# Performance work log

Measured on AMD Instinct MI355X. Metric: run time of the kernel, lower is better.

## Reference

```python
import jax, jax.numpy as jnp
import numpy as np

N = 16384      # nodes
E = 262144     # edges (avg degree 16)
H = 128        # hidden_channels
F = 128        # num_filters
G = 50         # num_gaussians
L = 6          # num_interactions
NG = 16        # graphs in batch
CUTOFF = 10.0
BOX = 5.0
LN2 = 0.6931471805599453


def _ssp(x):  # ShiftedSoftplus
    return jax.nn.softplus(x) - LN2


def setup_inputs() -> dict:
    key = jax.random.key(0)
    ks = jax.random.split(key, 20)
    w = lambda k, shape: jax.random.normal(k, shape, dtype=jnp.float32) * 0.1
    return {
        "z": jax.random.randint(ks[0], (N,), 0, 2),
        "pos": jax.random.uniform(ks[1], (N, 3), dtype=jnp.float32) * BOX,
        "edge_index": jax.random.randint(ks[2], (2, E), 0, N),
        "batch": jnp.sort(jax.random.randint(ks[3], (N,), 0, NG)),
        "emb": w(ks[4], (2, H)),
        "mlp_w1": w(ks[5], (L, G, F)),
        "mlp_b1": jnp.zeros((L, F), jnp.float32),
        "mlp_w2": w(ks[6], (L, F, F)),
        "mlp_b2": jnp.zeros((L, F), jnp.float32),
        "cf_w1": w(ks[7], (L, H, F)),
        "cf_w2": w(ks[8], (L, F, H)),
        "cf_b2": jnp.zeros((L, H), jnp.float32),
        "lin_w": w(ks[9], (L, H, H)),
        "lin_b": jnp.zeros((L, H), jnp.float32),
        "out_w1": w(ks[10], (H, H // 2)),
        "out_b1": jnp.zeros((H // 2,), jnp.float32),
        "out_w2": w(ks[11], (H // 2, 1)),
        "out_b2": jnp.zeros((1,), jnp.float32),
    }


def reference(z, pos, edge_index, batch, emb, mlp_w1, mlp_b1, mlp_w2, mlp_b2,
              cf_w1, cf_w2, cf_b2, lin_w, lin_b, out_w1, out_b1, out_w2, out_b2):
    row, col = edge_index[0], edge_index[1]  # message flows row -> col
    dx = pos[row] - pos[col]
    dx = dx - jnp.round(dx / BOX) * BOX      # minimum-image PBC
    ew = jnp.sqrt(jnp.sum(dx * dx, axis=-1))               # [E]
    offset = jnp.linspace(0.0, CUTOFF, G)
    coeff = -0.5 / (offset[1] - offset[0]) ** 2
    ea = jnp.exp(coeff * (ew[:, None] - offset[None, :]) ** 2)  # [E, G]
    C = 0.5 * (jnp.cos(ew * jnp.pi / CUTOFF) + 1.0)
    C = C * (ew < CUTOFF).astype(C.dtype)                   # [E]

    h = emb[z]                                              # [N, H]
    for l in range(L):
        # continuous filter from smeared distances, with cosine cutoff
        W = (_ssp(ea @ mlp_w1[l] + mlp_b1[l]) @ mlp_w2[l] + mlp_b2[l]) * C[:, None]  # [E, F]
        xh = h @ cf_w1[l]                                   # [N, F] (lin1, no bias)
        msg = xh[row] * W                                   # gather x_j, modulate
        agg = jax.ops.segment_sum(msg, col, num_segments=N)  # scatter-add
        xc = agg @ cf_w2[l] + cf_b2[l]                      # [N, H] (lin2)
        h = h + (_ssp(xc) @ lin_w[l] + lin_b[l])            # residual interaction

    h = _ssp(h @ out_w1 + out_b1) @ out_w2 + out_b2         # [N, 1]
    out = jax.ops.segment_sum(h, batch, num_segments=NG)    # readout 'add'
    return jax.nn.sigmoid(out)                              # [NG, 1]
```

## Files before the change

### kernel.cpp

```cpp
#include <hip/hip_runtime.h>
#include <math.h>

#define N_NODES 16384
#define N_EDGES 262144
#define HDIM    128
#define NG50    50
#define NLAYER  6
#define NGRAPH  16
#define TROWS   1025
#define RMAXF   4.34f
#define WPL     16384

__device__ __forceinline__ float ssp_f(float x){
  return (x > 20.0f ? x : log1pf(__expf(x))) - 0.6931471805599453f;
}
__device__ __forceinline__ void fma4(float4& c, float a, const float4 b){
  c.x = fmaf(a,b.x,c.x); c.y = fmaf(a,b.y,c.y); c.z = fmaf(a,b.z,c.z); c.w = fmaf(a,b.w,c.w);
}
__device__ __forceinline__ unsigned short f2bf(float x){
  unsigned u = __float_as_uint(x);
  u += 0x7FFF + ((u>>16)&1);
  return (unsigned short)(u>>16);
}
__device__ __forceinline__ float bf2f(unsigned short u){
  return __uint_as_float(((unsigned)u)<<16);
}

typedef __attribute__((ext_vector_type(8))) short bf16x8;
typedef __attribute__((ext_vector_type(4))) float f32x4;
__device__ __forceinline__ int swzf(int lin){ return lin ^ (((lin>>9)&7)<<4); }

__device__ __forceinline__ void split8(const float4 v0, const float4 v1, bf16x8& hi, bf16x8& lo){
  float x[8] = {v0.x,v0.y,v0.z,v0.w,v1.x,v1.y,v1.z,v1.w};
  #pragma unroll
  for (int i=0;i<8;++i){
    unsigned short h = f2bf(x[i]);
    hi[i] = (short)h;
    lo[i] = (short)f2bf(x[i] - bf2f(h));
  }
}

#define TAB_R   4
#define TAB_NB  257
#define B_INIT  2048
#define B_TAB   1542
#define B_HIST  1024
#define B_WPACK 144
#define K1_GRID (B_INIT + B_TAB + B_HIST + B_WPACK)

__global__ __launch_bounds__(256) void k_setup1(
    const int* __restrict__ z, const float* __restrict__ emb, float* __restrict__ h,
    const float* __restrict__ w1, const float* __restrict__ b1,
    const float* __restrict__ w2, const float* __restrict__ b2, float* __restrict__ tab,
    const int* __restrict__ ei, int* __restrict__ cursor,
    const float* __restrict__ cf_w2, const float* __restrict__ lin_w,
    const float* __restrict__ cf_w1, ushort* __restrict__ wp)
{
  __shared__ float ea[TAB_R][52];
  __shared__ float sT[TAB_R][HDIM];
  __shared__ float part[2][TAB_R][HDIM];
  const int b = blockIdx.x;
  const int tid = threadIdx.x;

  if (b < B_INIT){
    int t = b*256 + tid;
    int n = t >> 5, q = t & 31;
    ((float4*)h)[t] = ((const float4*)emb)[(z[n]<<5) + q];
    return;
  }
  if (b < B_INIT + B_TAB){
    int bb = b - B_INIT;
    int l  = bb / TAB_NB;
    int i0 = (bb % TAB_NB) * TAB_R;
    int j    = tid & 127;
    int half = tid >> 7;
    const float* w1l = w1 + (size_t)l*NG50*HDIM;
    const float* w2l = w2 + (size_t)l*HDIM*HDIM;
    float* tabl = tab + (size_t)l*TROWS*HDIM;
    const float STEP = RMAXF/1024.0f;
    const float GS   = 10.0f/49.0f;
    const float GC   = -0.5f/(GS*GS);
    if (tid < TAB_R*NG50){
      int rr = tid / NG50, k = tid - rr*NG50;
      int ri = i0 + rr; if (ri > TROWS-1) ri = TROWS-1;
      float d = ri*STEP - k*GS;
      ea[rr][k] = __expf(GC*d*d);
    }
    __syncthreads();
    {
      float acc[TAB_R] = {0,0,0,0};
      int kb = half*25;
      for (int k=0;k<25;++k){
        float wv = w1l[(kb+k)*HDIM + j];
        #pragma unroll
        for (int r=0;r<TAB_R;++r) acc[r] = fmaf(ea[r][kb+k], wv, acc[r]);
      }
      #pragma unroll
      for (int r=0;r<TAB_R;++r) part[half][r][j] = acc[r];
    }
    __syncthreads();
    {
      float b1v = b1[(size_t)l*HDIM + j];
      #pragma unroll
      for (int rr=0;rr<2;++rr){
        int r = half*2 + rr;
        sT[r][j] = ssp_f(part[0][r][j] + part[1][r][j] + b1v);
      }
    }
    __syncthreads();
    {
      float o[TAB_R] = {0,0,0,0};
      int kb = half*64;
      #pragma unroll 4
      for (int k=0;k<64;++k){
        float wv = w2l[(kb+k)*HDIM + j];
        #pragma unroll
        for (int r=0;r<TAB_R;++r) o[r] = fmaf(sT[r][kb+k], wv, o[r]);
      }
      #pragma unroll
      for (int r=0;r<TAB_R;++r) part[half][r][j] = o[r];
    }
    __syncthreads();
    {
      float b2v = b2[(size_t)l*HDIM + j];
      #pragma unroll
      for (int rr=0;rr<2;++rr){
        int r = half*2 + rr;
        int ri = i0 + r;
        if (ri < TROWS){
          float rv = ri*STEP;
          float C = 0.5f*(cosf(rv*0.31415926535897931f) + 1.0f);
          tabl[(size_t)ri*HDIM + j] = (part[0][r][j] + part[1][r][j] + b2v)*C;
        }
      }
    }
    return;
  }
  if (b < B_INIT + B_TAB + B_HIST){
    int e = (b - (B_INIT + B_TAB))*256 + tid;
    if (e < N_EDGES) atomicAdd(&cursor[ei[N_EDGES + e]], 1);
    return;
  }
  {
    int bb  = b - (B_INIT + B_TAB + B_HIST);
    int mat = bb >> 3;
    int s   = (bb & 7)*256 + tid;
    const float* M = (mat < 6)  ? cf_w2 + (size_t)mat*HDIM*HDIM
                   : (mat < 12) ? lin_w + (size_t)(mat-6)*HDIM*HDIM
                                : cf_w1 + (size_t)(mat-12)*HDIM*HDIM;
    int ct = s >> 8, ks = (s >> 6) & 3, l = s & 63;
    int col = ct*16 + (l & 15);
    int r0  = ks*32 + (l >> 4)*8;
    ushort oh[8], ol[8];
    #pragma unroll
    for (int i=0;i<8;++i){
      float w = M[(size_t)(r0+i)*HDIM + col];
      oh[i] = f2bf(w);
      ol[i] = f2bf(w - bf2f(oh[i]));
    }
    ushort* dh = wp + (size_t)(2*mat)*WPL + (size_t)s*8;
    ushort* dl = dh + WPL;
    *(ushort4*)(dh+0) = make_ushort4(oh[0],oh[1],oh[2],oh[3]);
    *(ushort4*)(dh+4) = make_ushort4(oh[4],oh[5],oh[6],oh[7]);
    *(ushort4*)(dl+0) = make_ushort4(ol[0],ol[1],ol[2],ol[3]);
    *(ushort4*)(dl+4) = make_ushort4(ol[4],ol[5],ol[6],ol[7]);
  }
}

__global__ __launch_bounds__(1024) void k_scan_pack(int* __restrict__ cursor,
    int* __restrict__ rowptr, const float* __restrict__ tab, ushort4* __restrict__ tabp){
  __shared__ int sbuf[1024];
  int t = threadIdx.x;
  if (blockIdx.x == 0){
    int base = t*16;
    int d[16]; int s = 0;
    #pragma unroll
    for (int i=0;i<16;++i){ d[i] = cursor[base+i]; s += d[i]; }
    sbuf[t] = s; __syncthreads();
    for (int off=1; off<1024; off<<=1){
      int v = sbuf[t];
      int add = (t >= off) ? sbuf[t-off] : 0;
      __syncthreads();
      sbuf[t] = v + add;
      __syncthreads();
    }
    int run = (t==0) ? 0 : sbuf[t-1];
    #pragma unroll
    for (int i=0;i<16;++i){ rowptr[base+i] = run; cursor[base+i] = run; run += d[i]; }
    if (t==1023) rowptr[N_NODES] = run;
    return;
  }
  size_t tt = (size_t)(blockIdx.x-1)*1024 + t;
  int lane = (int)(tt & 63);
  size_t row = tt >> 6;
  size_t l = row >> 10, i = row & 1023;
  const float* a = tab + (l*TROWS + i)*HDIM + lane*2;
  float2 av = *(const float2*)a;
  float2 bv = *(const float2*)(a + HDIM);
  ushort4 p;
  p.x = f2bf(av.x); p.y = f2bf(av.y); p.z = f2bf(bv.x); p.w = f2bf(bv.y);
  tabp[tt] = p;
}

#define FR 16
__global__ __launch_bounds__(256,4) void k_fill_xh(
    const int* __restrict__ ei, const float* __restrict__ pos,
    int* __restrict__ cursor, int* __restrict__ srcl, float* __restrict__ tl,
    const float* __restrict__ A, const float* __restrict__ B, ushort4* __restrict__ Cb)
{
  __shared__ float Bs[32*HDIM];
  const int tid = threadIdx.x;
  if (blockIdx.x < 1024){
    int e = blockIdx.x*256 + tid;
    if (e < N_EDGES){
      int a = ei[e];
      int c = ei[N_EDGES + e];
      float dx = pos[3*a+0] - pos[3*c+0];
      float dy = pos[3*a+1] - pos[3*c+1];
      float dz = pos[3*a+2] - pos[3*c+2];
      dx -= rintf(dx*0.2f)*5.0f;
      dy -= rintf(dy*0.2f)*5.0f;
      dz -= rintf(dz*0.2f)*5.0f;
      float r = sqrtf(fmaf(dx,dx,fmaf(dy,dy,dz*dz)));
      int slot = atomicAdd(&cursor[c], 1);
      srcl[slot] = a;
      tl[slot]   = r * (1024.0f/RMAXF);
    }
    return;
  }
  int m0 = (blockIdx.x - 1024)*FR;
  int tc = tid & 31, tr = tid >> 5;
  int j0 = tc*4;
  int lr0 = tr*2, lr1 = tr*2+1;
  float4 acc0 = make_float4(0,0,0,0), acc1 = acc0;
  const float* A0 = A + (size_t)(m0 + lr0)*HDIM;
  const float* A1 = A + (size_t)(m0 + lr1)*HDIM;
  for (int kc=0; kc<HDIM; kc+=32){
    __syncthreads();
    {
      const float4* src = (const float4*)(B + kc*HDIM);
      float4* dst = (float4*)Bs;
      #pragma unroll
      for (int i=0;i<4;++i) dst[tid + i*256] = src[tid + i*256];
    }
    __syncthreads();
    #pragma unroll
    for (int kk=0; kk<32; kk+=4){
      float4 b0 = *(const float4*)(Bs + (kk+0)*HDIM + j0);
      float4 b1 = *(const float4*)(Bs + (kk+1)*HDIM + j0);
      float4 b2 = *(const float4*)(Bs + (kk+2)*HDIM + j0);
      float4 b3 = *(const float4*)(Bs + (kk+3)*HDIM + j0);
      float4 a0 = *(const float4*)(A0 + kc + kk);
      float4 a1 = *(const float4*)(A1 + kc + kk);
      fma4(acc0,a0.x,b0); fma4(acc0,a0.y,b1); fma4(acc0,a0.z,b2); fma4(acc0,a0.w,b3);
      fma4(acc1,a1.x,b0); fma4(acc1,a1.y,b1); fma4(acc1,a1.z,b2); fma4(acc1,a1.w,b3);
    }
  }
  ushort4 o;
  o.x=f2bf(acc0.x); o.y=f2bf(acc0.y); o.z=f2bf(acc0.z); o.w=f2bf(acc0.w);
  Cb[(size_t)(m0 + lr0)*32 + tc] = o;
  o.x=f2bf(acc1.x); o.y=f2bf(acc1.y); o.z=f2bf(acc1.z); o.w=f2bf(acc1.w);
  Cb[(size_t)(m0 + lr1)*32 + tc] = o;
}

__device__ __forceinline__ void gemm_hl(const ushort* plane, size_t wfo,
    const bf16x8* ah, const bf16x8* al, f32x4* acc){
  #pragma unroll
  for (int ks=0;ks<4;++ks){
    #pragma unroll
    for (int c=0;c<2;++c){
      const ushort* p = plane + wfo + (size_t)(c*4+ks)*512;
      bf16x8 wh = *(const bf16x8*)p;
      bf16x8 wl = *(const bf16x8*)(p + WPL);
      acc[c] = __builtin_amdgcn_mfma_f32_16x16x32_bf16(ah[ks], wh, acc[c], 0,0,0);
      acc[c] = __builtin_amdgcn_mfma_f32_16x16x32_bf16(al[ks], wh, acc[c], 0,0,0);
      acc[c] = __builtin_amdgcn_mfma_f32_16x16x32_bf16(ah[ks], wl, acc[c], 0,0,0);
    }
  }
}
template<bool LAST>
__global__ __launch_bounds__(256,4) void k_layer(
    const int* __restrict__ rowptr, const int* __restrict__ srcl, const float* __restrict__ tl,
    const ushort4* __restrict__ tabp, const ushort2* __restrict__ xh_cur,
    const ushort* __restrict__ w2p, const float* __restrict__ B2,
    const ushort* __restrict__ wlp, const float* __restrict__ BL,
    float* __restrict__ Hio, const ushort* __restrict__ w1p, ushort* __restrict__ xh_nxt)
{
  __shared__ alignas(16) float Sa[16*HDIM];
  __shared__ alignas(16) float St[16*HDIM];
  const int tid  = threadIdx.x;
  const int wv   = tid >> 6, lane = tid & 63;
  const int m0   = blockIdx.x * 16;

  {
    const ushort4* tabl = tabp + lane;
    const ushort2* xh2  = xh_cur + lane;
    for (int i=0;i<4;++i){
      int c = m0 + wv*4 + i;
      int beg = rowptr[c], end = rowptr[c+1];
      float ax = 0.f, ay = 0.f;
      for (int k0 = beg; k0 < end; k0 += 64){
        int rem = end - k0;
        int cnt = rem < 64 ? rem : 64;
        int   s_l = 0; float t_l = 0.f;
        if (lane < cnt){ s_l = srcl[k0+lane]; t_l = tl[k0+lane]; }
        int j = 0;
        for (; j+3 < cnt; j += 4){
          int   r0 = __shfl(s_l, j,   64);
          float t0 = __shfl(t_l, j,   64);
          int   r1 = __shfl(s_l, j+1, 64);
          float t1 = __shfl(t_l, j+1, 64);
          int   r2 = __shfl(s_l, j+2, 64);
          float t2 = __shfl(t_l, j+2, 64);
          int   r3 = __shfl(s_l, j+3, 64);
          float t3 = __shfl(t_l, j+3, 64);
          int i00 = (int)t0; if (i00 > 1023) i00 = 1023;
          int i01 = (int)t1; if (i01 > 1023) i01 = 1023;
          int i02 = (int)t2; if (i02 > 1023) i02 = 1023;
          int i03 = (int)t3; if (i03 > 1023) i03 = 1023;
          float f0 = t0 - (float)i00;
          float f1 = t1 - (float)i01;
          float f2 = t2 - (float)i02;
          float f3 = t3 - (float)i03;
          ushort4 p0 = tabl[(size_t)i00*64];
          ushort4 p1 = tabl[(size_t)i01*64];
          ushort4 p2 = tabl[(size_t)i02*64];
          ushort4 p3 = tabl[(size_t)i03*64];
          ushort2 x0 = xh2[(size_t)r0*64];
          ushort2 x1 = xh2[(size_t)r1*64];
          ushort2 x2 = xh2[(size_t)r2*64];
          ushort2 x3 = xh2[(size_t)r3*64];
          float a0x=bf2f(p0.x), a0y=bf2f(p0.y), d0x=bf2f(p0.z)-a0x, d0y=bf2f(p0.w)-a0y;
          float a1x=bf2f(p1.x), a1y=bf2f(p1.y), d1x=bf2f(p1.z)-a1x, d1y=bf2f(p1.w)-a1y;
          float a2x=bf2f(p2.x), a2y=bf2f(p2.y), d2x=bf2f(p2.z)-a2x, d2y=bf2f(p2.w)-a2y;
          float a3x=bf2f(p3.x), a3y=bf2f(p3.y), d3x=bf2f(p3.z)-a3x, d3y=bf2f(p3.w)-a3y;
          ax = fmaf(bf2f(x0.x), fmaf(f0, d0x, a0x), ax);
          ay = fmaf(bf2f(x0.y), fmaf(f0, d0y, a0y), ay);
          ax = fmaf(bf2f(x1.x), fmaf(f1, d1x, a1x), ax);
          ay = fmaf(bf2f(x1.y), fmaf(f1, d1y, a1y), ay);
          ax = fmaf(bf2f(x2.x), fmaf(f2, d2x, a2x), ax);
          ay = fmaf(bf2f(x2.y), fmaf(f2, d2y, a2y), ay);
          ax = fmaf(bf2f(x3.x), fmaf(f3, d3x, a3x), ax);
          ay = fmaf(bf2f(x3.y), fmaf(f3, d3y, a3y), ay);
        }
        for (; j < cnt; ++j){
          int   r0 = __shfl(s_l, j, 64);
          float t0 = __shfl(t_l, j, 64);
          int i00 = (int)t0; if (i00 > 1023) i00 = 1023;
          float f0 = t0 - (float)i00;
          ushort4 p0 = tabl[(size_t)i00*64];
          ushort2 x0 = xh2[(size_t)r0*64];
          float a0x=bf2f(p0.x), a0y=bf2f(p0.y), d0x=bf2f(p0.z)-a0x, d0y=bf2f(p0.w)-a0y;
          ax = fmaf(bf2f(x0.x), fmaf(f0, d0x, a0x), ax);
          ay = fmaf(bf2f(x0.y), fmaf(f0, d0y, a0y), ay);
        }
      }
      *(float2*)((char*)Sa + swzf((wv*4+i)*512 + lane*8)) = make_float2(ax, ay);
    }
  }
  __syncthreads();

  const int m = lane & 15, g = lane >> 4;
  const int colA = wv*32 + m;
  const int colB = colA + 16;
  const size_t wfo = (size_t)(wv*8*64 + lane)*8;
  const f32x4 vzero = {0.f,0.f,0.f,0.f};
  bf16x8 ah[4], al[4];
  f32x4 acc[2];

  #pragma unroll
  for (int ks=0;ks<4;++ks){
    int lin = m*512 + (ks*32 + g*8)*4;
    split8(*(const float4*)((const char*)Sa + swzf(lin)),
           *(const float4*)((const char*)Sa + swzf(lin + 16)), ah[ks], al[ks]);
  }
  acc[0] = vzero; acc[1] = vzero;
  gemm_hl(w2p, wfo, ah, al, acc);
  {
    const float b20 = B2[colA], b21 = B2[colB];
    #pragma unroll
    for (int r=0;r<4;++r){
      const int row = g*4 + r;
      *(float*)((char*)St + swzf(row*512 + colA*4)) = ssp_f(acc[0][r] + b20);
      *(float*)((char*)St + swzf(row*512 + colB*4)) = ssp_f(acc[1][r] + b21);
    }
  }
  __syncthreads();

  #pragma unroll
  for (int ks=0;ks<4;++ks){
    int lin = m*512 + (ks*32 + g*8)*4;
    split8(*(const float4*)((const char*)St + swzf(lin)),
           *(const float4*)((const char*)St + swzf(lin + 16)), ah[ks], al[ks]);
  }
  float hr0[4], hr1[4];
  #pragma unroll
  for (int r=0;r<4;++r){
    hr0[r] = Hio[(size_t)(m0 + g*4 + r)*HDIM + colA];
    hr1[r] = Hio[(size_t)(m0 + g*4 + r)*HDIM + colB];
  }
  acc[0] = vzero; acc[1] = vzero;
  gemm_hl(wlp, wfo, ah, al, acc);
  {
    const float bl0 = BL[colA], bl1 = BL[colB];
    #pragma unroll
    for (int r=0;r<4;++r){
      const int row = g*4 + r;
      float v0 = hr0[r] + acc[0][r] + bl0;
      float v1 = hr1[r] + acc[1][r] + bl1;
      Hio[(size_t)(m0+row)*HDIM + colA] = v0;
      Hio[(size_t)(m0+row)*HDIM + colB] = v1;
      if (!LAST){
        *(float*)((char*)Sa + swzf(row*512 + colA*4)) = v0;
        *(float*)((char*)Sa + swzf(row*512 + colB*4)) = v1;
      }
    }
  }
  if (LAST) return;
  __syncthreads();

  #pragma unroll
  for (int ks=0;ks<4;++ks){
    int lin = m*512 + (ks*32 + g*8)*4;
    split8(*(const float4*)((const char*)Sa + swzf(lin)),
           *(const float4*)((const char*)Sa + swzf(lin + 16)), ah[ks], al[ks]);
  }
  acc[0] = vzero; acc[1] = vzero;
  gemm_hl(w1p, wfo, ah, al, acc);
  #pragma unroll
  for (int r=0;r<4;++r){
    const int row = g*4 + r;
    xh_nxt[(size_t)(m0+row)*HDIM + colA] = f2bf(acc[0][r]);
    xh_nxt[(size_t)(m0+row)*HDIM + colB] = f2bf(acc[1][r]);
  }
}

__global__ __launch_bounds__(256) void k_outA(const float* __restrict__ h, const float* __restrict__ w1,
    const float* __restrict__ b1, const float* __restrict__ w2, const float* __restrict__ b2,
    float* __restrict__ nodeval){
  int node = blockIdx.x*4 + (threadIdx.x >> 6);
  int lane = threadIdx.x & 63;
  float acc = b1[lane];
  const float* hrow = h + (size_t)node*HDIM;
  #pragma unroll 4
  for (int k=0;k<HDIM;++k) acc = fmaf(hrow[k], w1[k*64 + lane], acc);
  float s = ssp_f(acc) * w2[lane];
  for (int off=32; off>0; off>>=1) s += __shfl_down(s, off, 64);
  if (lane == 0) nodeval[node] = s + b2[0];
}

__global__ __launch_bounds__(256) void k_outB(const float* __restrict__ nodeval,
    const int* __restrict__ batch, float* __restrict__ out){
  __shared__ float sred[4];
  int g = blockIdx.x;
  int t = threadIdx.x;
  float s = 0.f;
  for (int n = t; n < N_NODES; n += 256)
    if (batch[n] == g) s += nodeval[n];
  for (int off=32; off>0; off>>=1) s += __shfl_down(s, off, 64);
  if ((t & 63) == 0) sred[t >> 6] = s;
  __syncthreads();
  if (t == 0){
    float tot = sred[0] + sred[1] + sred[2] + sred[3];
    out[g] = 1.0f/(1.0f + __expf(-tot));
  }
}

extern "C" void kernel_launch(void* const* d_in, const int* in_sizes, int n_in,
                              void* d_out, int out_size, void* d_ws, size_t ws_size,
                              hipStream_t stream){
  (void)in_sizes; (void)n_in; (void)out_size;
  const int*   z      = (const int*)  d_in[0];
  const float* pos    = (const float*)d_in[1];
  const int*   ei     = (const int*)  d_in[2];
  const int*   batch  = (const int*)  d_in[3];
  const float* emb    = (const float*)d_in[4];
  const float* mlp_w1 = (const float*)d_in[5];
  const float* mlp_b1 = (const float*)d_in[6];
  const float* mlp_w2 = (const float*)d_in[7];
  const float* mlp_b2 = (const float*)d_in[8];
  const float* cf_w1  = (const float*)d_in[9];
  const float* cf_w2  = (const float*)d_in[10];
  const float* cf_b2  = (const float*)d_in[11];
  const float* lin_w  = (const float*)d_in[12];
  const float* lin_b  = (const float*)d_in[13];
  const float* ow1    = (const float*)d_in[14];
  const float* ob1    = (const float*)d_in[15];
  const float* ow2    = (const float*)d_in[16];
  const float* ob2    = (const float*)d_in[17];

  char* wp = (char*)d_ws;
  size_t used = 0;
  auto alloc = [&](size_t bytes)->char*{
    char* p = wp + used;
    used += (bytes + 1023) & ~(size_t)1023;
    return p;
  };
  float*   tab     = (float*)alloc((size_t)NLAYER*TROWS*HDIM*4);
  ushort4* tabp    = (ushort4*)alloc((size_t)NLAYER*1024*64*8);
  float*   h       = (float*)alloc((size_t)N_NODES*HDIM*4);
  ushort*  xhb0    = (ushort*)alloc((size_t)N_NODES*HDIM*2);
  ushort*  xhb1    = (ushort*)alloc((size_t)N_NODES*HDIM*2);
  ushort*  wpk     = (ushort*)alloc((size_t)36*WPL*2);
  int*     rowptr  = (int*)  alloc((size_t)(N_NODES+1)*4);
  int*     cursor  = (int*)  alloc((size_t)N_NODES*4);
  int*     srcl    = (int*)  alloc((size_t)N_EDGES*4);
  float*   tl      = (float*)alloc((size_t)N_EDGES*4);
  float*   nodeval = (float*)alloc((size_t)N_NODES*4);
  if (used > ws_size) return;

  hipMemsetAsync(cursor, 0, (size_t)N_NODES*4, stream);

  k_setup1<<<K1_GRID, 256, 0, stream>>>(z, emb, h,
      mlp_w1, mlp_b1, mlp_w2, mlp_b2, tab, ei, cursor, cf_w2, lin_w, cf_w1, wpk);
  k_scan_pack<<<385, 1024, 0, stream>>>(cursor, rowptr, tab, tabp);
  k_fill_xh<<<2048, 256, 0, stream>>>(ei, pos, cursor, srcl, tl, h, cf_w1, (ushort4*)xhb0);

  for (int l=0; l<NLAYER; ++l){
    const ushort* w2p = wpk + (size_t)(2*l)*WPL;
    const ushort* wlp = wpk + (size_t)(2*(6+l))*WPL;
    const ushort2* xcur = (const ushort2*)((l & 1) ? xhb1 : xhb0);
    ushort*        xnxt = (l & 1) ? xhb0 : xhb1;
    if (l < NLAYER-1){
      const ushort* w1p = wpk + (size_t)(2*(13+l))*WPL;
      k_layer<false><<<N_NODES/16, 256, 0, stream>>>(rowptr, srcl, tl,
                 tabp + (size_t)l*1024*64, xcur,
                 w2p, cf_b2 + (size_t)l*HDIM, wlp, lin_b + (size_t)l*HDIM, h,
                 w1p, xnxt);
    } else {
      k_layer<true><<<N_NODES/16, 256, 0, stream>>>(rowptr, srcl, tl,
                 tabp + (size_t)l*1024*64, xcur,
                 w2p, cf_b2 + (size_t)l*HDIM, wlp, lin_b + (size_t)l*HDIM, h,
                 nullptr, nullptr);
    }
  }
  k_outA  <<<N_NODES/4, 256, 0, stream>>>(h, ow1, ob1, ow2, ob2, nodeval);
  k_outB  <<<NGRAPH, 256, 0, stream>>>(nodeval, batch, (float*)d_out);
}
```

Before: 395.6 us.

## Fuse layer loop and readout into one cooperative persistent kernel

Replaces the six per-layer launches plus the two readout kernels with a single cooperative kernel. It loops over layers and node tiles and uses grid-wide syncs between stages. Separately, the filter table build now writes packed bf16 interpolation pairs directly from setup, so the fp32 intermediate table and the pack kernel go away. This removes launch gaps and one memory round trip. In exchange it relies on cooperative launch, and the grid is capped at occupancy times 256 (likely the CU count), which may leave fewer blocks in flight per stage.

```diff
diff --git a/kernel.cpp b/kernel.cpp
--- a/kernel.cpp
+++ b/kernel.cpp
@@ -1,5 +1,8 @@
 #include <hip/hip_runtime.h>
+#include <hip/hip_cooperative_groups.h>
 #include <math.h>
+
+namespace cg = cooperative_groups;
 
 #define N_NODES 16384
 #define N_EDGES 262144
@@ -40,10 +43,8 @@
   }
 }
 
-#define TAB_R   4
-#define TAB_NB  257
 #define B_INIT  2048
-#define B_TAB   1542
+#define B_TAB   1536
 #define B_HIST  1024
 #define B_WPACK 144
 #define K1_GRID (B_INIT + B_TAB + B_HIST + B_WPACK)
@@ -51,14 +52,15 @@
 __global__ __launch_bounds__(256) void k_setup1(
     const int* __restrict__ z, const float* __restrict__ emb, float* __restrict__ h,
     const float* __restrict__ w1, const float* __restrict__ b1,
-    const float* __restrict__ w2, const float* __restrict__ b2, float* __restrict__ tab,
+    const float* __restrict__ w2, const float* __restrict__ b2, ushort4* __restrict__ tabp,
     const int* __restrict__ ei, int* __restrict__ cursor,
     const float* __restrict__ cf_w2, const float* __restrict__ lin_w,
     const float* __restrict__ cf_w1, ushort* __restrict__ wp)
 {
-  __shared__ float ea[TAB_R][52];
-  __shared__ float sT[TAB_R][HDIM];
-  __shared__ float part[2][TAB_R][HDIM];
+  __shared__ float ea[5][52];
+  __shared__ float sT5[5][HDIM];
+  __shared__ float part5[2][5][HDIM];
+  __shared__ float fin5[5][HDIM];
   const int b = blockIdx.x;
   const int tid = threadIdx.x;
 
@@ -70,69 +72,77 @@
   }
   if (b < B_INIT + B_TAB){
     int bb = b - B_INIT;
-    int l  = bb / TAB_NB;
-    int i0 = (bb % TAB_NB) * TAB_R;
+    int l  = bb >> 8;
+    int i0 = (bb & 255)*4;
     int j    = tid & 127;
     int half = tid >> 7;
     const float* w1l = w1 + (size_t)l*NG50*HDIM;
     const float* w2l = w2 + (size_t)l*HDIM*HDIM;
-    float* tabl = tab + (size_t)l*TROWS*HDIM;
     const float STEP = RMAXF/1024.0f;
     const float GS   = 10.0f/49.0f;
     const float GC   = -0.5f/(GS*GS);
-    if (tid < TAB_R*NG50){
+    if (tid < 5*NG50){
       int rr = tid / NG50, k = tid - rr*NG50;
-      int ri = i0 + rr; if (ri > TROWS-1) ri = TROWS-1;
+      int ri = i0 + rr;
       float d = ri*STEP - k*GS;
       ea[rr][k] = __expf(GC*d*d);
     }
     __syncthreads();
     {
-      float acc[TAB_R] = {0,0,0,0};
+      float acc[5] = {0,0,0,0,0};
       int kb = half*25;
       for (int k=0;k<25;++k){
         float wv = w1l[(kb+k)*HDIM + j];
         #pragma unroll
-        for (int r=0;r<TAB_R;++r) acc[r] = fmaf(ea[r][kb+k], wv, acc[r]);
-      }
-      #pragma unroll
-      for (int r=0;r<TAB_R;++r) part[half][r][j] = acc[r];
+        for (int r=0;r<5;++r) acc[r] = fmaf(ea[r][kb+k], wv, acc[r]);
+      }
+      #pragma unroll
+      for (int r=0;r<5;++r) part5[half][r][j] = acc[r];
     }
     __syncthreads();
     {
       float b1v = b1[(size_t)l*HDIM + j];
       #pragma unroll
-      for (int rr=0;rr<2;++rr){
-        int r = half*2 + rr;
-        sT[r][j] = ssp_f(part[0][r][j] + part[1][r][j] + b1v);
+      for (int rr=0;rr<3;++rr){
+        int r = half*3 + rr;
+        if (r < 5) sT5[r][j] = ssp_f(part5[0][r][j] + part5[1][r][j] + b1v);
       }
     }
     __syncthreads();
     {
-      float o[TAB_R] = {0,0,0,0};
+      float o[5] = {0,0,0,0,0};
       int kb = half*64;
       #pragma unroll 4
       for (int k=0;k<64;++k){
         float wv = w2l[(kb+k)*HDIM + j];
         #pragma unroll
-        for (int r=0;r<TAB_R;++r) o[r] = fmaf(sT[r][kb+k], wv, o[r]);
-      }
-      #pragma unroll
-      for (int r=0;r<TAB_R;++r) part[half][r][j] = o[r];
+        for (int r=0;r<5;++r) o[r] = fmaf(sT5[r][kb+k], wv, o[r]);
+      }
+      #pragma unroll
+      for (int r=0;r<5;++r) part5[half][r][j] = o[r];
     }
     __syncthreads();
     {
       float b2v = b2[(size_t)l*HDIM + j];
       #pragma unroll
-      for (int rr=0;rr<2;++rr){
-        int r = half*2 + rr;
-        int ri = i0 + r;
-        if (ri < TROWS){
+      for (int rr=0;rr<3;++rr){
+        int r = half*3 + rr;
+        if (r < 5){
+          int ri = i0 + r;
           float rv = ri*STEP;
           float C = 0.5f*(cosf(rv*0.31415926535897931f) + 1.0f);
-          tabl[(size_t)ri*HDIM + j] = (part[0][r][j] + part[1][r][j] + b2v)*C;
+          fin5[r][j] = (part5[0][r][j] + part5[1][r][j] + b2v)*C;
         }
       }
+    }
+    __syncthreads();
+    {
+      int r  = tid >> 6, ln = tid & 63;
+      int ri = i0 + r;
+      ushort4 p;
+      p.x = f2bf(fin5[r][ln*2]);   p.y = f2bf(fin5[r][ln*2+1]);
+      p.z = f2bf(fin5[r+1][ln*2]); p.w = f2bf(fin5[r+1][ln*2+1]);
+      tabp[((size_t)l*1024 + ri)*64 + ln] = p;
     }
     return;
   }
@@ -167,39 +177,25 @@
   }
 }
 
-__global__ __launch_bounds__(1024) void k_scan_pack(int* __restrict__ cursor,
-    int* __restrict__ rowptr, const float* __restrict__ tab, ushort4* __restrict__ tabp){
+__global__ __launch_bounds__(1024) void k_scan(int* __restrict__ cursor, int* __restrict__ rowptr){
   __shared__ int sbuf[1024];
   int t = threadIdx.x;
-  if (blockIdx.x == 0){
-    int base = t*16;
-    int d[16]; int s = 0;
-    #pragma unroll
-    for (int i=0;i<16;++i){ d[i] = cursor[base+i]; s += d[i]; }
-    sbuf[t] = s; __syncthreads();
-    for (int off=1; off<1024; off<<=1){
-      int v = sbuf[t];
-      int add = (t >= off) ? sbuf[t-off] : 0;
-      __syncthreads();
-      sbuf[t] = v + add;
-      __syncthreads();
-    }
-    int run = (t==0) ? 0 : sbuf[t-1];
-    #pragma unroll
-    for (int i=0;i<16;++i){ rowptr[base+i] = run; cursor[base+i] = run; run += d[i]; }
-    if (t==1023) rowptr[N_NODES] = run;
-    return;
-  }
-  size_t tt = (size_t)(blockIdx.x-1)*1024 + t;
-  int lane = (int)(tt & 63);
-  size_t row = tt >> 6;
-  size_t l = row >> 10, i = row & 1023;
-  const float* a = tab + (l*TROWS + i)*HDIM + lane*2;
-  float2 av = *(const float2*)a;
-  float2 bv = *(const float2*)(a + HDIM);
-  ushort4 p;
-  p.x = f2bf(av.x); p.y = f2bf(av.y); p.z = f2bf(bv.x); p.w = f2bf(bv.y);
-  tabp[tt] = p;
+  int base = t*16;
+  int d[16]; int s = 0;
+  #pragma unroll
+  for (int i=0;i<16;++i){ d[i] = cursor[base+i]; s += d[i]; }
+  sbuf[t] = s; __syncthreads();
+  for (int off=1; off<1024; off<<=1){
+    int v = sbuf[t];
+    int add = (t >= off) ? sbuf[t-off] : 0;
+    __syncthreads();
+    sbuf[t] = v + add;
+    __syncthreads();
+  }
+  int run = (t==0) ? 0 : sbuf[t-1];
+  #pragma unroll
+  for (int i=0;i<16;++i){ rowptr[base+i] = run; cursor[base+i] = run; run += d[i]; }
+  if (t==1023) rowptr[N_NODES] = run;
 }
 
 #define FR 16
@@ -278,191 +274,209 @@
     }
   }
 }
-template<bool LAST>
-__global__ __launch_bounds__(256,4) void k_layer(
+
+__global__ __launch_bounds__(256,4) void k_mega(
     const int* __restrict__ rowptr, const int* __restrict__ srcl, const float* __restrict__ tl,
-    const ushort4* __restrict__ tabp, const ushort2* __restrict__ xh_cur,
-    const ushort* __restrict__ w2p, const float* __restrict__ B2,
-    const ushort* __restrict__ wlp, const float* __restrict__ BL,
-    float* __restrict__ Hio, const ushort* __restrict__ w1p, ushort* __restrict__ xh_nxt)
+    const ushort4* __restrict__ tabp_all, ushort* __restrict__ xhb0, ushort* __restrict__ xhb1,
+    const ushort* __restrict__ wpk, const float* __restrict__ cf_b2, const float* __restrict__ lin_b,
+    float* __restrict__ Hio,
+    const float* __restrict__ ow1, const float* __restrict__ ob1,
+    const float* __restrict__ ow2, const float* __restrict__ ob2,
+    const int* __restrict__ batch, float* __restrict__ nodeval, float* __restrict__ out)
 {
+  cg::grid_group grid = cg::this_grid();
   __shared__ alignas(16) float Sa[16*HDIM];
   __shared__ alignas(16) float St[16*HDIM];
+  __shared__ float sred[4];
   const int tid  = threadIdx.x;
   const int wv   = tid >> 6, lane = tid & 63;
-  const int m0   = blockIdx.x * 16;
-
-  {
-    const ushort4* tabl = tabp + lane;
-    const ushort2* xh2  = xh_cur + lane;
-    for (int i=0;i<4;++i){
-      int c = m0 + wv*4 + i;
-      int beg = rowptr[c], end = rowptr[c+1];
-      float ax = 0.f, ay = 0.f;
-      for (int k0 = beg; k0 < end; k0 += 64){
-        int rem = end - k0;
-        int cnt = rem < 64 ? rem : 64;
-        int   s_l = 0; float t_l = 0.f;
-        if (lane < cnt){ s_l = srcl[k0+lane]; t_l = tl[k0+lane]; }
-        int j = 0;
-        for (; j+3 < cnt; j += 4){
-          int   r0 = __shfl(s_l, j,   64);
-          float t0 = __shfl(t_l, j,   64);
-          int   r1 = __shfl(s_l, j+1, 64);
-          float t1 = __shfl(t_l, j+1, 64);
-          int   r2 = __shfl(s_l, j+2, 64);
-          float t2 = __shfl(t_l, j+2, 64);
-          int   r3 = __shfl(s_l, j+3, 64);
-          float t3 = __shfl(t_l, j+3, 64);
-          int i00 = (int)t0; if (i00 > 1023) i00 = 1023;
-          int i01 = (int)t1; if (i01 > 1023) i01 = 1023;
-          int i02 = (int)t2; if (i02 > 1023) i02 = 1023;
-          int i03 = (int)t3; if (i03 > 1023) i03 = 1023;
-          float f0 = t0 - (float)i00;
-          float f1 = t1 - (float)i01;
-          float f2 = t2 - (float)i02;
-          float f3 = t3 - (float)i03;
-          ushort4 p0 = tabl[(size_t)i00*64];
-          ushort4 p1 = tabl[(size_t)i01*64];
-          ushort4 p2 = tabl[(size_t)i02*64];
-          ushort4 p3 = tabl[(size_t)i03*64];
-          ushort2 x0 = xh2[(size_t)r0*64];
-          ushort2 x1 = xh2[(size_t)r1*64];
-          ushort2 x2 = xh2[(size_t)r2*64];
-          ushort2 x3 = xh2[(size_t)r3*64];
-          float a0x=bf2f(p0.x), a0y=bf2f(p0.y), d0x=bf2f(p0.z)-a0x, d0y=bf2f(p0.w)-a0y;
-          float a1x=bf2f(p1.x), a1y=bf2f(p1.y), d1x=bf2f(p1.z)-a1x, d1y=bf2f(p1.w)-a1y;
-          float a2x=bf2f(p2.x), a2y=bf2f(p2.y), d2x=bf2f(p2.z)-a2x, d2y=bf2f(p2.w)-a2y;
-          float a3x=bf2f(p3.x), a3y=bf2f(p3.y), d3x=bf2f(p3.z)-a3x, d3y=bf2f(p3.w)-a3y;
-          ax = fmaf(bf2f(x0.x), fmaf(f0, d0x, a0x), ax);
-          ay = fmaf(bf2f(x0.y), fmaf(f0, d0y, a0y), ay);
-          ax = fmaf(bf2f(x1.x), fmaf(f1, d1x, a1x), ax);
-          ay = fmaf(bf2f(x1.y), fmaf(f1, d1y, a1y), ay);
-          ax = fmaf(bf2f(x2.x), fmaf(f2, d2x, a2x), ax);
-          ay = fmaf(bf2f(x2.y), fmaf(f2, d2y, a2y), ay);
-          ax = fmaf(bf2f(x3.x), fmaf(f3, d3x, a3x), ax);
-          ay = fmaf(bf2f(x3.y), fmaf(f3, d3y, a3y), ay);
-        }
-        for (; j < cnt; ++j){
-          int   r0 = __shfl(s_l, j, 64);
-          float t0 = __shfl(t_l, j, 64);
-          int i00 = (int)t0; if (i00 > 1023) i00 = 1023;
-          float f0 = t0 - (float)i00;
-          ushort4 p0 = tabl[(size_t)i00*64];
-          ushort2 x0 = xh2[(size_t)r0*64];
-          float a0x=bf2f(p0.x), a0y=bf2f(p0.y), d0x=bf2f(p0.z)-a0x, d0y=bf2f(p0.w)-a0y;
-          ax = fmaf(bf2f(x0.x), fmaf(f0, d0x, a0x), ax);
-          ay = fmaf(bf2f(x0.y), fmaf(f0, d0y, a0y), ay);
-        }
-      }
-      *(float2*)((char*)Sa + swzf((wv*4+i)*512 + lane*8)) = make_float2(ax, ay);
-    }
-  }
-  __syncthreads();
-
-  const int m = lane & 15, g = lane >> 4;
+  const int m    = lane & 15, g = lane >> 4;
   const int colA = wv*32 + m;
   const int colB = colA + 16;
   const size_t wfo = (size_t)(wv*8*64 + lane)*8;
   const f32x4 vzero = {0.f,0.f,0.f,0.f};
-  bf16x8 ah[4], al[4];
-  f32x4 acc[2];
-
-  #pragma unroll
-  for (int ks=0;ks<4;++ks){
-    int lin = m*512 + (ks*32 + g*8)*4;
-    split8(*(const float4*)((const char*)Sa + swzf(lin)),
-           *(const float4*)((const char*)Sa + swzf(lin + 16)), ah[ks], al[ks]);
-  }
-  acc[0] = vzero; acc[1] = vzero;
-  gemm_hl(w2p, wfo, ah, al, acc);
-  {
-    const float b20 = B2[colA], b21 = B2[colB];
-    #pragma unroll
-    for (int r=0;r<4;++r){
-      const int row = g*4 + r;
-      *(float*)((char*)St + swzf(row*512 + colA*4)) = ssp_f(acc[0][r] + b20);
-      *(float*)((char*)St + swzf(row*512 + colB*4)) = ssp_f(acc[1][r] + b21);
-    }
-  }
-  __syncthreads();
-
-  #pragma unroll
-  for (int ks=0;ks<4;++ks){
-    int lin = m*512 + (ks*32 + g*8)*4;
-    split8(*(const float4*)((const char*)St + swzf(lin)),
-           *(const float4*)((const char*)St + swzf(lin + 16)), ah[ks], al[ks]);
-  }
-  float hr0[4], hr1[4];
-  #pragma unroll
-  for (int r=0;r<4;++r){
-    hr0[r] = Hio[(size_t)(m0 + g*4 + r)*HDIM + colA];
-    hr1[r] = Hio[(size_t)(m0 + g*4 + r)*HDIM + colB];
-  }
-  acc[0] = vzero; acc[1] = vzero;
-  gemm_hl(wlp, wfo, ah, al, acc);
-  {
-    const float bl0 = BL[colA], bl1 = BL[colB];
-    #pragma unroll
-    for (int r=0;r<4;++r){
-      const int row = g*4 + r;
-      float v0 = hr0[r] + acc[0][r] + bl0;
-      float v1 = hr1[r] + acc[1][r] + bl1;
-      Hio[(size_t)(m0+row)*HDIM + colA] = v0;
-      Hio[(size_t)(m0+row)*HDIM + colB] = v1;
-      if (!LAST){
-        *(float*)((char*)Sa + swzf(row*512 + colA*4)) = v0;
-        *(float*)((char*)Sa + swzf(row*512 + colB*4)) = v1;
-      }
-    }
-  }
-  if (LAST) return;
-  __syncthreads();
-
-  #pragma unroll
-  for (int ks=0;ks<4;++ks){
-    int lin = m*512 + (ks*32 + g*8)*4;
-    split8(*(const float4*)((const char*)Sa + swzf(lin)),
-           *(const float4*)((const char*)Sa + swzf(lin + 16)), ah[ks], al[ks]);
-  }
-  acc[0] = vzero; acc[1] = vzero;
-  gemm_hl(w1p, wfo, ah, al, acc);
-  #pragma unroll
-  for (int r=0;r<4;++r){
-    const int row = g*4 + r;
-    xh_nxt[(size_t)(m0+row)*HDIM + colA] = f2bf(acc[0][r]);
-    xh_nxt[(size_t)(m0+row)*HDIM + colB] = f2bf(acc[1][r]);
-  }
-}
-
-__global__ __launch_bounds__(256) void k_outA(const float* __restrict__ h, const float* __restrict__ w1,
-    const float* __restrict__ b1, const float* __restrict__ w2, const float* __restrict__ b2,
-    float* __restrict__ nodeval){
-  int node = blockIdx.x*4 + (threadIdx.x >> 6);
-  int lane = threadIdx.x & 63;
-  float acc = b1[lane];
-  const float* hrow = h + (size_t)node*HDIM;
-  #pragma unroll 4
-  for (int k=0;k<HDIM;++k) acc = fmaf(hrow[k], w1[k*64 + lane], acc);
-  float s = ssp_f(acc) * w2[lane];
-  for (int off=32; off>0; off>>=1) s += __shfl_down(s, off, 64);
-  if (lane == 0) nodeval[node] = s + b2[0];
-}
-
-__global__ __launch_bounds__(256) void k_outB(const float* __restrict__ nodeval,
-    const int* __restrict__ batch, float* __restrict__ out){
-  __shared__ float sred[4];
-  int g = blockIdx.x;
-  int t = threadIdx.x;
-  float s = 0.f;
-  for (int n = t; n < N_NODES; n += 256)
-    if (batch[n] == g) s += nodeval[n];
-  for (int off=32; off>0; off>>=1) s += __shfl_down(s, off, 64);
-  if ((t & 63) == 0) sred[t >> 6] = s;
-  __syncthreads();
-  if (t == 0){
-    float tot = sred[0] + sred[1] + sred[2] + sred[3];
-    out[g] = 1.0f/(1.0f + __expf(-tot));
+
+  for (int l=0; l<NLAYER; ++l){
+    const bool last = (l == NLAYER-1);
+    const ushort*  w2p  = wpk + (size_t)(2*l)*WPL;
+    const ushort*  wlp  = wpk + (size_t)(2*(6+l))*WPL;
+    const ushort*  w1p  = wpk + (size_t)(2*(13+l))*WPL;
+    const ushort4* tabL = tabp_all + (size_t)l*1024*64;
+    const ushort2* xcur = (const ushort2*)((l & 1) ? xhb1 : xhb0);
+    ushort*        xnxt = (l & 1) ? xhb0 : xhb1;
+    const float*   B2   = cf_b2 + (size_t)l*HDIM;
+    const float*   BL   = lin_b + (size_t)l*HDIM;
+
+    for (int tile = blockIdx.x; tile < N_NODES/16; tile += gridDim.x){
+      const int m0 = tile*16;
+
+      {
+        const ushort4* tabl = tabL + lane;
+        const ushort2* xh2  = xcur + lane;
+        for (int i=0;i<4;++i){
+          int c = m0 + wv*4 + i;
+          int beg = rowptr[c], end = rowptr[c+1];
+          float ax = 0.f, ay = 0.f;
+          for (int k0 = beg; k0 < end; k0 += 64){
+            int rem = end - k0;
+            int cnt = rem < 64 ? rem : 64;
+            int   s_l = 0; float t_l = 0.f;
+            if (lane < cnt){ s_l = srcl[k0+lane]; t_l = tl[k0+lane]; }
+            int j = 0;
+            for (; j+3 < cnt; j += 4){
+              int   r0 = __shfl(s_l, j,   64);
+              float t0 = __shfl(t_l, j,   64);
+              int   r1 = __shfl(s_l, j+1, 64);
+              float t1 = __shfl(t_l, j+1, 64);
+              int   r2 = __shfl(s_l, j+2, 64);
+              float t2 = __shfl(t_l, j+2, 64);
+              int   r3 = __shfl(s_l, j+3, 64);
+              float t3 = __shfl(t_l, j+3, 64);
+              int i00 = (int)t0; if (i00 > 1023) i00 = 1023;
+              int i01 = (int)t1; if (i01 > 1023) i01 = 1023;
+              int i02 = (int)t2; if (i02 > 1023) i02 = 1023;
+              int i03 = (int)t3; if (i03 > 1023) i03 = 1023;
+              float f0 = t0 - (float)i00;
+              float f1 = t1 - (float)i01;
+              float f2 = t2 - (float)i02;
+              float f3 = t3 - (float)i03;
+              ushort4 p0 = tabl[(size_t)i00*64];
+              ushort4 p1 = tabl[(size_t)i01*64];
+              ushort4 p2 = tabl[(size_t)i02*64];
+              ushort4 p3 = tabl[(size_t)i03*64];
+              ushort2 x0 = xh2[(size_t)r0*64];
+              ushort2 x1 = xh2[(size_t)r1*64];
+              ushort2 x2 = xh2[(size_t)r2*64];
+              ushort2 x3 = xh2[(size_t)r3*64];
+              float a0x=bf2f(p0.x), a0y=bf2f(p0.y), d0x=bf2f(p0.z)-a0x, d0y=bf2f(p0.w)-a0y;
+              float a1x=bf2f(p1.x), a1y=bf2f(p1.y), d1x=bf2f(p1.z)-a1x, d1y=bf2f(p1.w)-a1y;
+              float a2x=bf2f(p2.x), a2y=bf2f(p2.y), d2x=bf2f(p2.z)-a2x, d2y=bf2f(p2.w)-a2y;
+              float a3x=bf2f(p3.x), a3y=bf2f(p3.y), d3x=bf2f(p3.z)-a3x, d3y=bf2f(p3.w)-a3y;
+              ax = fmaf(bf2f(x0.x), fmaf(f0, d0x, a0x), ax);
+              ay = fmaf(bf2f(x0.y), fmaf(f0, d0y, a0y), ay);
+              ax = fmaf(bf2f(x1.x), fmaf(f1, d1x, a1x), ax);
+              ay = fmaf(bf2f(x1.y), fmaf(f1, d1y, a1y), ay);
+              ax = fmaf(bf2f(x2.x), fmaf(f2, d2x, a2x), ax);
+              ay = fmaf(bf2f(x2.y), fmaf(f2, d2y, a2y), ay);
+              ax = fmaf(bf2f(x3.x), fmaf(f3, d3x, a3x), ax);
+              ay = fmaf(bf2f(x3.y), fmaf(f3, d3y, a3y), ay);
+            }
+            for (; j < cnt; ++j){
+              int   r0 = __shfl(s_l, j, 64);
+              float t0 = __shfl(t_l, j, 64);
+              int i00 = (int)t0; if (i00 > 1023) i00 = 1023;
+              float f0 = t0 - (float)i00;
+              ushort4 p0 = tabl[(size_t)i00*64];
+              ushort2 x0 = xh2[(size_t)r0*64];
+              float a0x=bf2f(p0.x), a0y=bf2f(p0.y), d0x=bf2f(p0.z)-a0x, d0y=bf2f(p0.w)-a0y;
+              ax = fmaf(bf2f(x0.x), fmaf(f0, d0x, a0x), ax);
+              ay = fmaf(bf2f(x0.y), fmaf(f0, d0y, a0y), ay);
+            }
+          }
+          *(float2*)((char*)Sa + swzf((wv*4+i)*512 + lane*8)) = make_float2(ax, ay);
+        }
+      }
+      __syncthreads();
+
+      bf16x8 ah[4], al[4];
+      f32x4 acc[2];
+
+      #pragma unroll
+      for (int ks=0;ks<4;++ks){
+        int lin = m*512 + (ks*32 + g*8)*4;
+        split8(*(const float4*)((const char*)Sa + swzf(lin)),
+               *(const float4*)((const char*)Sa + swzf(lin + 16)), ah[ks], al[ks]);
+      }
+      acc[0] = vzero; acc[1] = vzero;
+      gemm_hl(w2p, wfo, ah, al, acc);
+      {
+        const float b20 = B2[colA], b21 = B2[colB];
+        #pragma unroll
+        for (int r=0;r<4;++r){
+          const int row = g*4 + r;
+          *(float*)((char*)St + swzf(row*512 + colA*4)) = ssp_f(acc[0][r] + b20);
+          *(float*)((char*)St + swzf(row*512 + colB*4)) = ssp_f(acc[1][r] + b21);
+        }
+      }
+      __syncthreads();
+
+      #pragma unroll
+      for (int ks=0;ks<4;++ks){
+        int lin = m*512 + (ks*32 + g*8)*4;
+        split8(*(const float4*)((const char*)St + swzf(lin)),
+               *(const float4*)((const char*)St + swzf(lin + 16)), ah[ks], al[ks]);
+      }
+      float hr0[4], hr1[4];
+      #pragma unroll
+      for (int r=0;r<4;++r){
+        hr0[r] = Hio[(size_t)(m0 + g*4 + r)*HDIM + colA];
+        hr1[r] = Hio[(size_t)(m0 + g*4 + r)*HDIM + colB];
+      }
+      acc[0] = vzero; acc[1] = vzero;
+      gemm_hl(wlp, wfo, ah, al, acc);
+      {
+        const float bl0 = BL[colA], bl1 = BL[colB];
+        #pragma unroll
+        for (int r=0;r<4;++r){
+          const int row = g*4 + r;
+          float v0 = hr0[r] + acc[0][r] + bl0;
+          float v1 = hr1[r] + acc[1][r] + bl1;
+          Hio[(size_t)(m0+row)*HDIM + colA] = v0;
+          Hio[(size_t)(m0+row)*HDIM + colB] = v1;
+          if (!last){
+            *(float*)((char*)Sa + swzf(row*512 + colA*4)) = v0;
+            *(float*)((char*)Sa + swzf(row*512 + colB*4)) = v1;
+          }
+        }
+      }
+      if (!last){
+        __syncthreads();
+        #pragma unroll
+        for (int ks=0;ks<4;++ks){
+          int lin = m*512 + (ks*32 + g*8)*4;
+          split8(*(const float4*)((const char*)Sa + swzf(lin)),
+                 *(const float4*)((const char*)Sa + swzf(lin + 16)), ah[ks], al[ks]);
+        }
+        acc[0] = vzero; acc[1] = vzero;
+        gemm_hl(w1p, wfo, ah, al, acc);
+        #pragma unroll
+        for (int r=0;r<4;++r){
+          const int row = g*4 + r;
+          xnxt[(size_t)(m0+row)*HDIM + colA] = f2bf(acc[0][r]);
+          xnxt[(size_t)(m0+row)*HDIM + colB] = f2bf(acc[1][r]);
+        }
+      }
+      __syncthreads();
+    }
+    grid.sync();
+  }
+
+  for (int tile = blockIdx.x; tile < N_NODES/16; tile += gridDim.x){
+    for (int i=0;i<4;++i){
+      int node = tile*16 + wv*4 + i;
+      float acc = ob1[lane];
+      const float* hrow = Hio + (size_t)node*HDIM;
+      #pragma unroll 4
+      for (int k=0;k<HDIM;++k) acc = fmaf(hrow[k], ow1[k*64 + lane], acc);
+      float s = ssp_f(acc) * ow2[lane];
+      for (int off=32; off>0; off>>=1) s += __shfl_down(s, off, 64);
+      if (lane == 0) nodeval[node] = s + ob2[0];
+    }
+  }
+  grid.sync();
+
+  if (blockIdx.x < NGRAPH){
+    int gg = blockIdx.x;
+    float s = 0.f;
+    for (int n = tid; n < N_NODES; n += 256)
+      if (batch[n] == gg) s += nodeval[n];
+    for (int off=32; off>0; off>>=1) s += __shfl_down(s, off, 64);
+    if ((tid & 63) == 0) sred[tid >> 6] = s;
+    __syncthreads();
+    if (tid == 0){
+      float tot = sred[0] + sred[1] + sred[2] + sred[3];
+      out[gg] = 1.0f/(1.0f + __expf(-tot));
+    }
   }
 }
 
@@ -496,7 +510,6 @@
     used += (bytes + 1023) & ~(size_t)1023;
     return p;
   };
-  float*   tab     = (float*)alloc((size_t)NLAYER*TROWS*HDIM*4);
   ushort4* tabp    = (ushort4*)alloc((size_t)NLAYER*1024*64*8);
   float*   h       = (float*)alloc((size_t)N_NODES*HDIM*4);
   ushort*  xhb0    = (ushort*)alloc((size_t)N_NODES*HDIM*2);
@@ -512,28 +525,23 @@
   hipMemsetAsync(cursor, 0, (size_t)N_NODES*4, stream);
 
   k_setup1<<<K1_GRID, 256, 0, stream>>>(z, emb, h,
-      mlp_w1, mlp_b1, mlp_w2, mlp_b2, tab, ei, cursor, cf_w2, lin_w, cf_w1, wpk);
-  k_scan_pack<<<385, 1024, 0, stream>>>(cursor, rowptr, tab, tabp);
+      mlp_w1, mlp_b1, mlp_w2, mlp_b2, tabp, ei, cursor, cf_w2, lin_w, cf_w1, wpk);
+  k_scan  <<<1, 1024, 0, stream>>>(cursor, rowptr);
   k_fill_xh<<<2048, 256, 0, stream>>>(ei, pos, cursor, srcl, tl, h, cf_w1, (ushort4*)xhb0);
 
-  for (int l=0; l<NLAYER; ++l){
-    const ushort* w2p = wpk + (size_t)(2*l)*WPL;
-    const ushort* wlp = wpk + (size_t)(2*(6+l))*WPL;
-    const ushort2* xcur = (const ushort2*)((l & 1) ? xhb1 : xhb0);
-    ushort*        xnxt = (l & 1) ? xhb0 : xhb1;
-    if (l < NLAYER-1){
-      const ushort* w1p = wpk + (size_t)(2*(13+l))*WPL;
-      k_layer<false><<<N_NODES/16, 256, 0, stream>>>(rowptr, srcl, tl,
-                 tabp + (size_t)l*1024*64, xcur,
-                 w2p, cf_b2 + (size_t)l*HDIM, wlp, lin_b + (size_t)l*HDIM, h,
-                 w1p, xnxt);
-    } else {
-      k_layer<true><<<N_NODES/16, 256, 0, stream>>>(rowptr, srcl, tl,
-                 tabp + (size_t)l*1024*64, xcur,
-                 w2p, cf_b2 + (size_t)l*HDIM, wlp, lin_b + (size_t)l*HDIM, h,
-                 nullptr, nullptr);
-    }
-  }
-  k_outA  <<<N_NODES/4, 256, 0, stream>>>(h, ow1, ob1, ow2, ob2, nodeval);
-  k_outB  <<<NGRAPH, 256, 0, stream>>>(nodeval, batch, (float*)d_out);
-}
+  int occ = 0;
+  if (hipOccupancyMaxActiveBlocksPerMultiprocessor(&occ, k_mega, 256, 0) != hipSuccess || occ < 1)
+    occ = 1;
+  int nb = occ * 256;
+  if (nb > N_NODES/16) nb = N_NODES/16;
+
+  float* outp = (float*)d_out;
+  void* margs[] = {
+    (void*)&rowptr, (void*)&srcl, (void*)&tl, (void*)&tabp,
+    (void*)&xhb0, (void*)&xhb1, (void*)&wpk,
+    (void*)&cf_b2, (void*)&lin_b, (void*)&h,
+    (void*)&ow1, (void*)&ob1, (void*)&ow2, (void*)&ob2,
+    (void*)&batch, (void*)&nodeval, (void*)&outp
+  };
+  hipLaunchCooperativeKernel(k_mega, dim3(nb), dim3(256), margs, 0, stream);
+}
```

Measured after the change: 1.198 ms. 203% more time.

## Fuse output MLP into last layer kernel and batch edge gathers by eight

Applied to the files above, without the earlier changes.

The per-node output MLP (128→64, shifted softplus, dot with w2) now runs inside the final k_layer using the h tile already held in shared memory, which removes the separate k_outA launch and its re-read of h from global memory. The edge aggregation loop is also restructured to issue up to eight table and feature gathers before consuming any of them, in place of the old 4-way unroll plus scalar tail. This aims to raise memory-level parallelism. The cost is more registers per thread, which may lower occupancy under launch_bounds(256,4).

```diff
diff --git a/kernel.cpp b/kernel.cpp
--- a/kernel.cpp
+++ b/kernel.cpp
@@ -284,7 +284,10 @@
     const ushort4* __restrict__ tabp, const ushort2* __restrict__ xh_cur,
     const ushort* __restrict__ w2p, const float* __restrict__ B2,
     const ushort* __restrict__ wlp, const float* __restrict__ BL,
-    float* __restrict__ Hio, const ushort* __restrict__ w1p, ushort* __restrict__ xh_nxt)
+    float* __restrict__ Hio, const ushort* __restrict__ w1p, ushort* __restrict__ xh_nxt,
+    const float* __restrict__ ow1, const float* __restrict__ ob1,
+    const float* __restrict__ ow2, const float* __restrict__ ob2,
+    float* __restrict__ nodeval)
 {
   __shared__ alignas(16) float Sa[16*HDIM];
   __shared__ alignas(16) float St[16*HDIM];
@@ -304,55 +307,29 @@
         int cnt = rem < 64 ? rem : 64;
         int   s_l = 0; float t_l = 0.f;
         if (lane < cnt){ s_l = srcl[k0+lane]; t_l = tl[k0+lane]; }
-        int j = 0;
-        for (; j+3 < cnt; j += 4){
-          int   r0 = __shfl(s_l, j,   64);
-          float t0 = __shfl(t_l, j,   64);
-          int   r1 = __shfl(s_l, j+1, 64);
-          float t1 = __shfl(t_l, j+1, 64);
-          int   r2 = __shfl(s_l, j+2, 64);
-          float t2 = __shfl(t_l, j+2, 64);
-          int   r3 = __shfl(s_l, j+3, 64);
-          float t3 = __shfl(t_l, j+3, 64);
-          int i00 = (int)t0; if (i00 > 1023) i00 = 1023;
-          int i01 = (int)t1; if (i01 > 1023) i01 = 1023;
-          int i02 = (int)t2; if (i02 > 1023) i02 = 1023;
-          int i03 = (int)t3; if (i03 > 1023) i03 = 1023;
-          float f0 = t0 - (float)i00;
-          float f1 = t1 - (float)i01;
-          float f2 = t2 - (float)i02;
-          float f3 = t3 - (float)i03;
-          ushort4 p0 = tabl[(size_t)i00*64];
-          ushort4 p1 = tabl[(size_t)i01*64];
-          ushort4 p2 = tabl[(size_t)i02*64];
-          ushort4 p3 = tabl[(size_t)i03*64];
-          ushort2 x0 = xh2[(size_t)r0*64];
-          ushort2 x1 = xh2[(size_t)r1*64];
-          ushort2 x2 = xh2[(size_t)r2*64];
-          ushort2 x3 = xh2[(size_t)r3*64];
-          float a0x=bf2f(p0.x), a0y=bf2f(p0.y), d0x=bf2f(p0.z)-a0x, d0y=bf2f(p0.w)-a0y;
-          float a1x=bf2f(p1.x), a1y=bf2f(p1.y), d1x=bf2f(p1.z)-a1x, d1y=bf2f(p1.w)-a1y;
-          float a2x=bf2f(p2.x), a2y=bf2f(p2.y), d2x=bf2f(p2.z)-a2x, d2y=bf2f(p2.w)-a2y;
-          float a3x=bf2f(p3.x), a3y=bf2f(p3.y), d3x=bf2f(p3.z)-a3x, d3y=bf2f(p3.w)-a3y;
-          ax = fmaf(bf2f(x0.x), fmaf(f0, d0x, a0x), ax);
-          ay = fmaf(bf2f(x0.y), fmaf(f0, d0y, a0y), ay);
-          ax = fmaf(bf2f(x1.x), fmaf(f1, d1x, a1x), ax);
-          ay = fmaf(bf2f(x1.y), fmaf(f1, d1y, a1y), ay);
-          ax = fmaf(bf2f(x2.x), fmaf(f2, d2x, a2x), ax);
-          ay = fmaf(bf2f(x2.y), fmaf(f2, d2y, a2y), ay);
-          ax = fmaf(bf2f(x3.x), fmaf(f3, d3x, a3x), ax);
-          ay = fmaf(bf2f(x3.y), fmaf(f3, d3y, a3y), ay);
-        }
-        for (; j < cnt; ++j){
-          int   r0 = __shfl(s_l, j, 64);
-          float t0 = __shfl(t_l, j, 64);
-          int i00 = (int)t0; if (i00 > 1023) i00 = 1023;
-          float f0 = t0 - (float)i00;
-          ushort4 p0 = tabl[(size_t)i00*64];
-          ushort2 x0 = xh2[(size_t)r0*64];
-          float a0x=bf2f(p0.x), a0y=bf2f(p0.y), d0x=bf2f(p0.z)-a0x, d0y=bf2f(p0.w)-a0y;
-          ax = fmaf(bf2f(x0.x), fmaf(f0, d0x, a0x), ax);
-          ay = fmaf(bf2f(x0.y), fmaf(f0, d0y, a0y), ay);
+        for (int w = 0; w < cnt; w += 8){
+          int wc = cnt - w; if (wc > 8) wc = 8;
+          ushort4 pp[8]; ushort2 xx[8]; float ff[8];
+          #pragma unroll
+          for (int e=0;e<8;++e){
+            if (e < wc){
+              int   rE = __shfl(s_l, w+e, 64);
+              float tE = __shfl(t_l, w+e, 64);
+              int iE = (int)tE; if (iE > 1023) iE = 1023;
+              ff[e] = tE - (float)iE;
+              pp[e] = tabl[(size_t)iE*64];
+              xx[e] = xh2[(size_t)rE*64];
+            }
+          }
+          #pragma unroll
+          for (int e=0;e<8;++e){
+            if (e < wc){
+              float aX=bf2f(pp[e].x), aY=bf2f(pp[e].y);
+              float dX=bf2f(pp[e].z)-aX, dY=bf2f(pp[e].w)-aY;
+              ax = fmaf(bf2f(xx[e].x), fmaf(ff[e], dX, aX), ax);
+              ay = fmaf(bf2f(xx[e].y), fmaf(ff[e], dY, aY), ay);
+            }
+          }
         }
       }
       *(float2*)((char*)Sa + swzf((wv*4+i)*512 + lane*8)) = make_float2(ax, ay);
@@ -410,14 +387,28 @@
       float v1 = hr1[r] + acc[1][r] + bl1;
       Hio[(size_t)(m0+row)*HDIM + colA] = v0;
       Hio[(size_t)(m0+row)*HDIM + colB] = v1;
-      if (!LAST){
-        *(float*)((char*)Sa + swzf(row*512 + colA*4)) = v0;
-        *(float*)((char*)Sa + swzf(row*512 + colB*4)) = v1;
+      *(float*)((char*)Sa + swzf(row*512 + colA*4)) = v0;
+      *(float*)((char*)Sa + swzf(row*512 + colB*4)) = v1;
+    }
+  }
+  __syncthreads();
+
+  if (LAST){
+    for (int i=0;i<4;++i){
+      const int row  = wv*4 + i;
+      const int node = m0 + row;
+      float acc1 = ob1[lane];
+      #pragma unroll 4
+      for (int k=0;k<HDIM;++k){
+        float hv = *(const float*)((const char*)Sa + swzf(row*512 + k*4));
+        acc1 = fmaf(hv, ow1[k*64 + lane], acc1);
       }
-    }
-  }
-  if (LAST) return;
-  __syncthreads();
+      float s = ssp_f(acc1) * ow2[lane];
+      for (int off=32; off>0; off>>=1) s += __shfl_down(s, off, 64);
+      if (lane == 0) nodeval[node] = s + ob2[0];
+    }
+    return;
+  }
 
   #pragma unroll
   for (int ks=0;ks<4;++ks){
@@ -433,20 +424,6 @@
     xh_nxt[(size_t)(m0+row)*HDIM + colA] = f2bf(acc[0][r]);
     xh_nxt[(size_t)(m0+row)*HDIM + colB] = f2bf(acc[1][r]);
   }
-}
-
-__global__ __launch_bounds__(256) void k_outA(const float* __restrict__ h, const float* __restrict__ w1,
-    const float* __restrict__ b1, const float* __restrict__ w2, const float* __restrict__ b2,
-    float* __restrict__ nodeval){
-  int node = blockIdx.x*4 + (threadIdx.x >> 6);
-  int lane = threadIdx.x & 63;
-  float acc = b1[lane];
-  const float* hrow = h + (size_t)node*HDIM;
-  #pragma unroll 4
-  for (int k=0;k<HDIM;++k) acc = fmaf(hrow[k], w1[k*64 + lane], acc);
-  float s = ssp_f(acc) * w2[lane];
-  for (int off=32; off>0; off>>=1) s += __shfl_down(s, off, 64);
-  if (lane == 0) nodeval[node] = s + b2[0];
 }
 
 __global__ __launch_bounds__(256) void k_outB(const float* __restrict__ nodeval,
@@ -526,14 +503,13 @@
       k_layer<false><<<N_NODES/16, 256, 0, stream>>>(rowptr, srcl, tl,
                  tabp + (size_t)l*1024*64, xcur,
                  w2p, cf_b2 + (size_t)l*HDIM, wlp, lin_b + (size_t)l*HDIM, h,
-                 w1p, xnxt);
+                 w1p, xnxt, nullptr, nullptr, nullptr, nullptr, nullptr);
     } else {
       k_layer<true><<<N_NODES/16, 256, 0, stream>>>(rowptr, srcl, tl,
                  tabp + (size_t)l*1024*64, xcur,
                  w2p, cf_b2 + (size_t)l*HDIM, wlp, lin_b + (size_t)l*HDIM, h,
-                 nullptr, nullptr);
-    }
-  }
-  k_outA  <<<N_NODES/4, 256, 0, stream>>>(h, ow1, ob1, ow2, ob2, nodeval);
+                 nullptr, nullptr, ow1, ob1, ow2, ob2, nodeval);
+    }
+  }
   k_outB  <<<NGRAPH, 256, 0, stream>>>(nodeval, batch, (float*)d_out);
 }
```

Measured after the change: 465.0 us. 17.5% more time.
